# Optimization experiments

Hardware: AMD Instinct MI355X
Metric: run time of the kernel (lower is better)

The kernel has to match this reference:

```python
import jax, jax.numpy as jnp
import numpy as np

B, L = 16384, 32
IN_DIM, TIME_DIM, HIDDEN, HEADS = 128, 64, 256, 4
HEAD_DIM = HIDDEN // HEADS
KV_DIM = IN_DIM + 2 * TIME_DIM
EPS = 1e-5


def setup_inputs() -> dict:
    key = jax.random.key(0)
    ks = jax.random.split(key, 16)
    s = lambda d: 1.0 / np.sqrt(d)
    return {
        "x_u": jax.random.normal(ks[0], (B, IN_DIM), jnp.float32),
        "x_ctx": jax.random.normal(ks[1], (B, L, IN_DIM), jnp.float32),
        "t_ctx": jax.random.uniform(ks[2], (B, L), jnp.float32) * 100.0,
        "freq": jax.random.normal(ks[3], (TIME_DIM,), jnp.float32),
        "phase": jnp.zeros((TIME_DIM,), jnp.float32),
        "Wq": jax.random.normal(ks[4], (IN_DIM, HIDDEN), jnp.float32) * s(IN_DIM),
        "Wk": jax.random.normal(ks[5], (KV_DIM, HIDDEN), jnp.float32) * s(KV_DIM),
        "Wv": jax.random.normal(ks[6], (KV_DIM, HIDDEN), jnp.float32) * s(KV_DIM),
        "Wres": jax.random.normal(ks[7], (IN_DIM, HIDDEN), jnp.float32) * s(IN_DIM),
        "bres": jnp.zeros((HIDDEN,), jnp.float32),
        "W1": jax.random.normal(ks[8], (HIDDEN, HIDDEN), jnp.float32) * s(HIDDEN),
        "b1": jnp.zeros((HIDDEN,), jnp.float32),
        "W2": jax.random.normal(ks[9], (HIDDEN, HIDDEN), jnp.float32) * s(HIDDEN),
        "b2": jnp.zeros((HIDDEN,), jnp.float32),
        "g1": jnp.ones((HIDDEN,), jnp.float32),
        "be1": jnp.zeros((HIDDEN,), jnp.float32),
        "g2": jnp.ones((HIDDEN,), jnp.float32),
        "be2": jnp.zeros((HIDDEN,), jnp.float32),
    }


def _layernorm(x, g, b):
    m = jnp.mean(x, axis=-1, keepdims=True)
    v = jnp.mean((x - m) ** 2, axis=-1, keepdims=True)
    return (x - m) * jax.lax.rsqrt(v + EPS) * g + b


def reference(x_u, x_ctx, t_ctx, freq, phase, Wq, Wk, Wv, Wres, bres,
              W1, b1, W2, b2, g1, be1, g2, be2):
    # --- time encoding: [B, L, 2*TIME_DIM]
    z = jnp.log1p(jnp.maximum(t_ctx, 0.0))[..., None] * freq + phase
    te = jnp.concatenate([jnp.sin(z), jnp.cos(z)], axis=-1)

    # --- single-query multi-head attention over L neighbors
    q = (x_u @ Wq).reshape(B, HEADS, HEAD_DIM)            # [B,H,d]
    kv = jnp.concatenate([x_ctx, te], axis=-1)            # [B,L,KV_DIM]
    k = (kv @ Wk).reshape(B, L, HEADS, HEAD_DIM)          # [B,L,H,d]
    v = (kv @ Wv).reshape(B, L, HEADS, HEAD_DIM)
    att = jnp.einsum('bhd,blhd->bhl', q, k) / np.sqrt(HEAD_DIM)
    att = jax.nn.softmax(att, axis=-1)                    # [B,H,L]
    agg = jnp.einsum('bhl,blhd->bhd', att, v).reshape(B, HIDDEN)

    # --- residual + norms + FFN (dropout is identity in eval)
    z1 = _layernorm(agg + x_u @ Wres + bres, g1, be1)
    ff = jax.nn.relu(z1 @ W1 + b1) @ W2 + b2
    return _layernorm(ff + z1, g2, be2)
```

## Files before the change

### kernel.cpp

```cpp
#include <hip/hip_runtime.h>

typedef unsigned short u16;
typedef unsigned int   u32;

using bf16x8 = __attribute__((ext_vector_type(8))) short;
using f32x4  = __attribute__((ext_vector_type(4))) float;

#define MFMA16(A, B, C) __builtin_amdgcn_mfma_f32_16x16x32_bf16((A), (B), (C), 0, 0, 0)

static __device__ __forceinline__ u16 f2b(float f) {
    u32 u = __builtin_bit_cast(u32, f);
    u32 r = (u + 0x7FFFu + ((u >> 16) & 1u)) >> 16;
    return (u16)r;
}
static __device__ __forceinline__ u16 f2bh(float f) {
    u32 u = __builtin_bit_cast(u32, f) + 0x8000u;
    return (u16)(u >> 16);
}
static __device__ __forceinline__ u32 pk2(float fa, float fb) {
    u32 a = __builtin_bit_cast(u32, fa) + 0x8000u;
    u32 b = __builtin_bit_cast(u32, fb) + 0x8000u;
    return __builtin_amdgcn_perm(b, a, 0x07060302u);
}
static __device__ __forceinline__ bf16x8 cvt8f(f32x4 a, f32x4 b) {
    union { u32 w[4]; bf16x8 v; } r;
    r.w[0] = pk2(a[0], a[1]); r.w[1] = pk2(a[2], a[3]);
    r.w[2] = pk2(b[0], b[1]); r.w[3] = pk2(b[2], b[3]);
    return r.v;
}
static __device__ __forceinline__ bf16x8 cvt8(f32x4 a, f32x4 b) {
    bf16x8 r;
    r[0] = (short)f2b(a[0]); r[1] = (short)f2b(a[1]);
    r[2] = (short)f2b(a[2]); r[3] = (short)f2b(a[3]);
    r[4] = (short)f2b(b[0]); r[5] = (short)f2b(b[1]);
    r[6] = (short)f2b(b[2]); r[7] = (short)f2b(b[3]);
    return r;
}

__global__ __launch_bounds__(256) void k0_prep(
    const float* __restrict__ Wq, const float* __restrict__ Wk,
    const float* __restrict__ Wv, const float* __restrict__ Wres,
    const float* __restrict__ W1, const float* __restrict__ W2,
    u16* __restrict__ WcatT, u16* __restrict__ WresT,
    u16* __restrict__ WvT, u16* __restrict__ W1T, u16* __restrict__ W2T)
{
    int t = blockIdx.x * 256 + threadIdx.x;
    if (t < 131072) {
        int n = t >> 7, i = t & 127;
        int h = n >> 8, c = n & 255;
        const float* wq = Wq + i * 256 + h * 64;
        const float* wk = Wk + c * 256 + h * 64;
        float acc = 0.f;
        #pragma unroll 8
        for (int d = 0; d < 64; ++d) acc += wq[d] * wk[d];
        WcatT[t] = f2b(acc * 0.125f);
    } else if (t < 163840) {
        int o = t - 131072; int n = o >> 7, i = o & 127;
        WresT[o] = f2b(Wres[i * 256 + n]);
    } else if (t < 229376) {
        int o = t - 163840; int n = o >> 8, c = o & 255;
        WvT[o] = f2b(Wv[c * 256 + n]);
    } else if (t < 294912) {
        int o = t - 229376; int n = o >> 8, c = o & 255;
        W1T[o] = f2b(W1[c * 256 + n]);
    } else {
        int o = t - 294912; int n = o >> 8, c = o & 255;
        W2T[o] = f2b(W2[c * 256 + n]);
    }
}

__global__ __launch_bounds__(256) void k1_qkvec(
    const float* __restrict__ xu, const u16* __restrict__ WcatT,
    u16* __restrict__ qkvec)
{
    __shared__ __align__(16) u16 As[128][136];
    const int m0 = blockIdx.x * 128, n0 = blockIdx.y * 128;
    const int t = threadIdx.x;
    #pragma unroll
    for (int i = 0; i < 8; ++i) {
        int c = t + i * 256;
        int row = c >> 4, ch = c & 15;
        const float* src = xu + (size_t)(m0 + row) * 128 + ch * 8;
        f32x4 a = *(const f32x4*)src;
        f32x4 b = *(const f32x4*)(src + 4);
        *(bf16x8*)&As[row][ch * 8] = cvt8(a, b);
    }
    __syncthreads();
    const int lane = t & 63, wave = t >> 6;
    const int quad = lane >> 4, l16 = lane & 15;
    const int mh = (wave >> 1) * 64, nh = (wave & 1) * 64;
    f32x4 zz = {0.f, 0.f, 0.f, 0.f};
    f32x4 acc[4][4];
    #pragma unroll
    for (int mt = 0; mt < 4; ++mt)
        #pragma unroll
        for (int nt = 0; nt < 4; ++nt) acc[mt][nt] = zz;
    #pragma unroll
    for (int ks = 0; ks < 4; ++ks) {
        bf16x8 a[4], b[4];
        #pragma unroll
        for (int mt = 0; mt < 4; ++mt)
            a[mt] = *(const bf16x8*)&As[mh + mt * 16 + l16][ks * 32 + quad * 8];
        #pragma unroll
        for (int nt = 0; nt < 4; ++nt)
            b[nt] = *(const bf16x8*)(WcatT + (size_t)(n0 + nh + nt * 16 + l16) * 128 + ks * 32 + quad * 8);
        #pragma unroll
        for (int mt = 0; mt < 4; ++mt)
            #pragma unroll
            for (int nt = 0; nt < 4; ++nt)
                acc[mt][nt] = MFMA16(a[mt], b[nt], acc[mt][nt]);
    }
    #pragma unroll
    for (int mt = 0; mt < 4; ++mt)
        #pragma unroll
        for (int nt = 0; nt < 4; ++nt) {
            int col = n0 + nh + nt * 16 + l16;
            #pragma unroll
            for (int r = 0; r < 4; ++r) {
                int row = m0 + mh + mt * 16 + quad * 4 + r;
                qkvec[(size_t)row * 1024 + col] = f2b(acc[mt][nt][r]);
            }
        }
}

__global__ __launch_bounds__(256) void k2_attn(
    const float* __restrict__ x_ctx, const float* __restrict__ t_ctx,
    const float* __restrict__ freq, const float* __restrict__ phase,
    u16* __restrict__ qkv)
{
    __shared__ __align__(16) u16 pw[4][4][32];
    const int t = threadIdx.x;
    const int lane = t & 63, wave = t >> 6;
    const int quad = lane >> 4, l16 = lane & 15;
    const int b = blockIdx.x * 4 + wave;
    const int fb = quad * 8;
    const f32x4 zz = {0.f, 0.f, 0.f, 0.f};

    float ltv = log1pf(fmaxf(t_ctx[(size_t)b * 32 + (lane & 31)], 0.f));

    f32x4 fr0a = *(const f32x4*)(freq + fb);
    f32x4 fr0b = *(const f32x4*)(freq + fb + 4);
    f32x4 fr1a = *(const f32x4*)(freq + 32 + fb);
    f32x4 fr1b = *(const f32x4*)(freq + 32 + fb + 4);
    f32x4 ph0a = *(const f32x4*)(phase + fb);
    f32x4 ph0b = *(const f32x4*)(phase + fb + 4);
    f32x4 ph1a = *(const f32x4*)(phase + 32 + fb);
    f32x4 ph1b = *(const f32x4*)(phase + 32 + fb + 4);

    const u16* qb = qkv + (size_t)b * 1024 + (size_t)(l16 & 3) * 256;

    f32x4 accA[2];
    #pragma unroll
    for (int ltile = 0; ltile < 2; ++ltile) {
        const int l = ltile * 16 + l16;
        const float* xrow = x_ctx + ((size_t)b * 32 + l) * 128;
        f32x4 acc = zz;
        #pragma unroll
        for (int ks = 0; ks < 4; ++ks) {
            f32x4 a = *(const f32x4*)(xrow + ks * 32 + fb);
            f32x4 c = *(const f32x4*)(xrow + ks * 32 + fb + 4);
            bf16x8 afr = cvt8f(a, c);
            bf16x8 bfr = *(const bf16x8*)(qb + ks * 32 + fb);
            acc = MFMA16(afr, bfr, acc);
        }
        float lt_l = __shfl(ltv, l);
        f32x4 z0a = fr0a * lt_l + ph0a;
        f32x4 z0b = fr0b * lt_l + ph0b;
        f32x4 z1a = fr1a * lt_l + ph1a;
        f32x4 z1b = fr1b * lt_l + ph1b;
        f32x4 s0a, s0b, s1a, s1b, c0a, c0b, c1a, c1b;
        #pragma unroll
        for (int j = 0; j < 4; ++j) {
            s0a[j] = __sinf(z0a[j]); s0b[j] = __sinf(z0b[j]);
            s1a[j] = __sinf(z1a[j]); s1b[j] = __sinf(z1b[j]);
            c0a[j] = __cosf(z0a[j]); c0b[j] = __cosf(z0b[j]);
            c1a[j] = __cosf(z1a[j]); c1b[j] = __cosf(z1b[j]);
        }
        acc = MFMA16(cvt8f(s0a, s0b), *(const bf16x8*)(qb + 128 + fb), acc);
        acc = MFMA16(cvt8f(s1a, s1b), *(const bf16x8*)(qb + 160 + fb), acc);
        acc = MFMA16(cvt8f(c0a, c0b), *(const bf16x8*)(qb + 192 + fb), acc);
        acc = MFMA16(cvt8f(c1a, c1b), *(const bf16x8*)(qb + 224 + fb), acc);
        accA[ltile] = acc;
    }

    float m = accA[0][0];
    #pragma unroll
    for (int r = 1; r < 4; ++r) m = fmaxf(m, accA[0][r]);
    #pragma unroll
    for (int r = 0; r < 4; ++r) m = fmaxf(m, accA[1][r]);
    m = fmaxf(m, __shfl_xor(m, 16));
    m = fmaxf(m, __shfl_xor(m, 32));
    float p[2][4], s = 0.f;
    #pragma unroll
    for (int lt2 = 0; lt2 < 2; ++lt2)
        #pragma unroll
        for (int r = 0; r < 4; ++r) { p[lt2][r] = __expf(accA[lt2][r] - m); s += p[lt2][r]; }
    s += __shfl_xor(s, 16);
    s += __shfl_xor(s, 32);
    float inv = 1.f / s;
    if (l16 < 4) {
        #pragma unroll
        for (int lt2 = 0; lt2 < 2; ++lt2)
            #pragma unroll
            for (int r = 0; r < 4; ++r)
                pw[wave][l16][lt2 * 16 + quad * 4 + r] = f2bh(p[lt2][r] * inv);
    }
    __syncthreads();

    bf16x8 pfr = *(const bf16x8*)&pw[wave][l16 & 3][fb];
    float ltj[8];
    #pragma unroll
    for (int j = 0; j < 8; ++j) ltj[j] = __shfl(ltv, fb + j);

    u16* crow = qkv + (size_t)b * 1024;
    #pragma unroll
    for (int nt = 0; nt < 8; ++nt) {
        int c = nt * 16 + l16;
        const float* xp = x_ctx + ((size_t)b * 32 + fb) * 128 + c;
        float v0 = xp[0], v1 = xp[128], v2 = xp[256], v3 = xp[384];
        float v4 = xp[512], v5 = xp[640], v6 = xp[768], v7 = xp[896];
        union { u32 w[4]; bf16x8 v; } bu;
        bu.w[0] = pk2(v0, v1); bu.w[1] = pk2(v2, v3);
        bu.w[2] = pk2(v4, v5); bu.w[3] = pk2(v6, v7);
        f32x4 d = MFMA16(pfr, bu.v, zz);
        if (quad == 0) {
            #pragma unroll
            for (int r = 0; r < 4; ++r) crow[r * 256 + c] = f2bh(d[r]);
        }
    }
    #pragma unroll
    for (int pp = 0; pp < 4; ++pp) {
        int f = pp * 16 + l16;
        float fq = freq[f], phf = phase[f];
        float z8[8];
        #pragma unroll
        for (int j = 0; j < 8; ++j) z8[j] = ltj[j] * fq + phf;
        union { u32 w[4]; bf16x8 v; } bs, bc;
        #pragma unroll
        for (int j = 0; j < 4; ++j) {
            bs.w[j] = pk2(__sinf(z8[2 * j]), __sinf(z8[2 * j + 1]));
            bc.w[j] = pk2(__cosf(z8[2 * j]), __cosf(z8[2 * j + 1]));
        }
        f32x4 ds = MFMA16(pfr, bs.v, zz);
        f32x4 dc = MFMA16(pfr, bc.v, zz);
        if (quad == 0) {
            #pragma unroll
            for (int r = 0; r < 4; ++r) {
                crow[r * 256 + 128 + f] = f2bh(ds[r]);
                crow[r * 256 + 192 + f] = f2bh(dc[r]);
            }
        }
    }
}

__global__ __launch_bounds__(256) void k3_epilogue(
    const u16* __restrict__ ctxb, const float* __restrict__ xu,
    const u16* __restrict__ WvT, const u16* __restrict__ WresT,
    const u16* __restrict__ W1T, const u16* __restrict__ W2T,
    const float* __restrict__ bres, const float* __restrict__ b1,
    const float* __restrict__ b2, const float* __restrict__ g1,
    const float* __restrict__ be1, const float* __restrict__ g2,
    const float* __restrict__ be2, float* __restrict__ out)
{
    __shared__ __align__(16) char smem[39552];
    u16  (*ctxs)[1032] = reinterpret_cast<u16 (*)[1032]>(smem);
    u16  (*xus)[136]   = reinterpret_cast<u16 (*)[136]>(smem + 33024);
    float(*zbuf)[264]  = reinterpret_cast<float (*)[264]>(smem);
    u16  (*z1b)[264]   = reinterpret_cast<u16 (*)[264]>(smem + 16896);
    u16  (*h1b)[264]   = reinterpret_cast<u16 (*)[264]>(smem + 25344);
    float(*obuf)[264]  = reinterpret_cast<float (*)[264]>(smem + 16896);
    float(*red)[16][2] = reinterpret_cast<float (*)[16][2]>(smem + 37376);
    float(*mrstd)[2]   = reinterpret_cast<float (*)[2]>(smem + 39424);

    const int b0 = blockIdx.x * 16;
    const int t = threadIdx.x;
    const int lane = t & 63, wave = t >> 6;
    const int quad = lane >> 4, l16 = lane & 15;
    const int nw = wave * 64;

    #pragma unroll
    for (int i = 0; i < 8; ++i) {
        int idx = t + i * 256;
        int row = idx >> 7, ch = idx & 127;
        *(bf16x8*)&ctxs[row][ch * 8] = *(const bf16x8*)(ctxb + (size_t)(b0 + row) * 1024 + ch * 8);
    }
    {
        int row = t >> 4, ch = t & 15;
        const float* src = xu + (size_t)(b0 + row) * 128 + ch * 8;
        f32x4 a = *(const f32x4*)src;
        f32x4 b = *(const f32x4*)(src + 4);
        *(bf16x8*)&xus[row][ch * 8] = cvt8(a, b);
    }
    __syncthreads();

    f32x4 zz = {0.f, 0.f, 0.f, 0.f};

    f32x4 acc[4];
    #pragma unroll
    for (int nt = 0; nt < 4; ++nt) acc[nt] = zz;
    #pragma unroll
    for (int ks = 0; ks < 8; ++ks) {
        bf16x8 afr = *(const bf16x8*)&ctxs[l16][wave * 256 + ks * 32 + quad * 8];
        #pragma unroll
        for (int nt = 0; nt < 4; ++nt) {
            bf16x8 bfr = *(const bf16x8*)(WvT + (size_t)(nw + nt * 16 + l16) * 256 + ks * 32 + quad * 8);
            acc[nt] = MFMA16(afr, bfr, acc[nt]);
        }
    }
    #pragma unroll
    for (int ks = 0; ks < 4; ++ks) {
        bf16x8 afr = *(const bf16x8*)&xus[l16][ks * 32 + quad * 8];
        #pragma unroll
        for (int nt = 0; nt < 4; ++nt) {
            bf16x8 bfr = *(const bf16x8*)(WresT + (size_t)(nw + nt * 16 + l16) * 128 + ks * 32 + quad * 8);
            acc[nt] = MFMA16(afr, bfr, acc[nt]);
        }
    }
    __syncthreads();
    #pragma unroll
    for (int nt = 0; nt < 4; ++nt) {
        int col = nw + nt * 16 + l16;
        float bb = bres[col];
        #pragma unroll
        for (int r = 0; r < 4; ++r)
            zbuf[quad * 4 + r][col] = acc[nt][r] + bb;
    }
    __syncthreads();

    {
        int row = t >> 4, j = t & 15;
        float s = 0.f, s2 = 0.f;
        #pragma unroll
        for (int i = 0; i < 16; ++i) { float v = zbuf[row][j + 16 * i]; s += v; s2 += v * v; }
        red[row][j][0] = s; red[row][j][1] = s2;
    }
    __syncthreads();
    if (t < 16) {
        float s = 0.f, s2 = 0.f;
        #pragma unroll
        for (int j = 0; j < 16; ++j) { s += red[t][j][0]; s2 += red[t][j][1]; }
        float m = s * (1.f / 256.f);
        float var = s2 * (1.f / 256.f) - m * m;
        mrstd[t][0] = m;
        mrstd[t][1] = rsqrtf(var + 1e-5f);
    }
    __syncthreads();
    {
        float g = g1[t], be = be1[t];
        #pragma unroll
        for (int i = 0; i < 16; ++i) {
            float z = (zbuf[i][t] - mrstd[i][0]) * mrstd[i][1] * g + be;
            zbuf[i][t] = z;
            z1b[i][t] = f2b(z);
        }
    }
    __syncthreads();

    f32x4 acc2[4];
    #pragma unroll
    for (int nt = 0; nt < 4; ++nt) acc2[nt] = zz;
    #pragma unroll
    for (int ks = 0; ks < 8; ++ks) {
        bf16x8 afr = *(const bf16x8*)&z1b[l16][ks * 32 + quad * 8];
        #pragma unroll
        for (int nt = 0; nt < 4; ++nt) {
            bf16x8 bfr = *(const bf16x8*)(W1T + (size_t)(nw + nt * 16 + l16) * 256 + ks * 32 + quad * 8);
            acc2[nt] = MFMA16(afr, bfr, acc2[nt]);
        }
    }
    #pragma unroll
    for (int nt = 0; nt < 4; ++nt) {
        int col = nw + nt * 16 + l16;
        float bb = b1[col];
        #pragma unroll
        for (int r = 0; r < 4; ++r)
            h1b[quad * 4 + r][col] = f2b(fmaxf(acc2[nt][r] + bb, 0.f));
    }
    __syncthreads();

    f32x4 acc3[4];
    #pragma unroll
    for (int nt = 0; nt < 4; ++nt) acc3[nt] = zz;
    #pragma unroll
    for (int ks = 0; ks < 8; ++ks) {
        bf16x8 afr = *(const bf16x8*)&h1b[l16][ks * 32 + quad * 8];
        #pragma unroll
        for (int nt = 0; nt < 4; ++nt) {
            bf16x8 bfr = *(const bf16x8*)(W2T + (size_t)(nw + nt * 16 + l16) * 256 + ks * 32 + quad * 8);
            acc3[nt] = MFMA16(afr, bfr, acc3[nt]);
        }
    }
    __syncthreads();
    #pragma unroll
    for (int nt = 0; nt < 4; ++nt) {
        int col = nw + nt * 16 + l16;
        float bb = b2[col];
        #pragma unroll
        for (int r = 0; r < 4; ++r) {
            int row = quad * 4 + r;
            obuf[row][col] = acc3[nt][r] + bb + zbuf[row][col];
        }
    }
    __syncthreads();

    {
        int row = t >> 4, j = t & 15;
        float s = 0.f, s2 = 0.f;
        #pragma unroll
        for (int i = 0; i < 16; ++i) { float v = obuf[row][j + 16 * i]; s += v; s2 += v * v; }
        red[row][j][0] = s; red[row][j][1] = s2;
    }
    __syncthreads();
    if (t < 16) {
        float s = 0.f, s2 = 0.f;
        #pragma unroll
        for (int j = 0; j < 16; ++j) { s += red[t][j][0]; s2 += red[t][j][1]; }
        float m = s * (1.f / 256.f);
        float var = s2 * (1.f / 256.f) - m * m;
        mrstd[t][0] = m;
        mrstd[t][1] = rsqrtf(var + 1e-5f);
    }
    __syncthreads();
    {
        float g = g2[t], be = be2[t];
        #pragma unroll
        for (int i = 0; i < 16; ++i)
            out[(size_t)(b0 + i) * 256 + t] = (obuf[i][t] - mrstd[i][0]) * mrstd[i][1] * g + be;
    }
}

extern "C" void kernel_launch(void* const* d_in, const int* in_sizes, int n_in,
                              void* d_out, int out_size, void* d_ws, size_t ws_size,
                              hipStream_t stream)
{
    (void)in_sizes; (void)n_in; (void)out_size; (void)ws_size;
    const float* xu    = (const float*)d_in[0];
    const float* x_ctx = (const float*)d_in[1];
    const float* t_ctx = (const float*)d_in[2];
    const float* freq  = (const float*)d_in[3];
    const float* phase = (const float*)d_in[4];
    const float* Wq    = (const float*)d_in[5];
    const float* Wk    = (const float*)d_in[6];
    const float* Wv    = (const float*)d_in[7];
    const float* Wres  = (const float*)d_in[8];
    const float* bres  = (const float*)d_in[9];
    const float* W1    = (const float*)d_in[10];
    const float* b1    = (const float*)d_in[11];
    const float* W2    = (const float*)d_in[12];
    const float* b2    = (const float*)d_in[13];
    const float* g1    = (const float*)d_in[14];
    const float* be1   = (const float*)d_in[15];
    const float* g2    = (const float*)d_in[16];
    const float* be2   = (const float*)d_in[17];
    float* out = (float*)d_out;

    char* ws = (char*)d_ws;
    u16* qkv   = (u16*)(ws);
    u16* WcatT = (u16*)(ws + 33554432);
    u16* WresT = (u16*)(ws + 33816576);
    u16* WvT   = (u16*)(ws + 33882112);
    u16* W1T   = (u16*)(ws + 34013184);
    u16* W2T   = (u16*)(ws + 34144256);

    hipLaunchKernelGGL(k0_prep, dim3(1408), dim3(256), 0, stream,
                       Wq, Wk, Wv, Wres, W1, W2, WcatT, WresT, WvT, W1T, W2T);
    hipLaunchKernelGGL(k1_qkvec, dim3(128, 8), dim3(256), 0, stream,
                       xu, WcatT, qkv);
    hipLaunchKernelGGL(k2_attn, dim3(4096), dim3(256), 0, stream,
                       x_ctx, t_ctx, freq, phase, qkv);
    hipLaunchKernelGGL(k3_epilogue, dim3(1024), dim3(256), 0, stream,
                       qkv, xu, WvT, WresT, W1T, W2T,
                       bres, b1, b2, g1, be1, g2, be2, out);
}
```

Baseline: 502.9 us.

## Fuse q-projection, attention, and epilogue kernels into one per-block kernel

Merges the q·Wk projection, the attention/context kernel and the epilogue into a single kernel. Each block handles 16 batch rows and keeps the per-row qk vectors and attention contexts in shared memory instead of writing them to and reading them back from a 32 MB global workspace. This removes two kernel launches and the global round-trip of the intermediate buffer. In exchange there are fewer blocks (1024 instead of 4096) for the memory-bound x_ctx streaming phase, each wave now loops over 4 rows with a block-wide barrier per iteration, and the shared-memory footprint grows.

```diff
diff --git a/kernel.cpp b/kernel.cpp
--- a/kernel.cpp
+++ b/kernel.cpp
@@ -69,74 +69,59 @@
     }
 }
 
-__global__ __launch_bounds__(256) void k1_qkvec(
-    const float* __restrict__ xu, const u16* __restrict__ WcatT,
-    u16* __restrict__ qkvec)
+__global__ __launch_bounds__(256, 4) void kf_fused(
+    const float* __restrict__ xu, const float* __restrict__ x_ctx,
+    const float* __restrict__ t_ctx, const float* __restrict__ freq,
+    const float* __restrict__ phase,
+    const u16* __restrict__ WcatT, const u16* __restrict__ WvT,
+    const u16* __restrict__ WresT, const u16* __restrict__ W1T,
+    const u16* __restrict__ W2T,
+    const float* __restrict__ bres, const float* __restrict__ b1,
+    const float* __restrict__ b2, const float* __restrict__ g1,
+    const float* __restrict__ be1, const float* __restrict__ g2,
+    const float* __restrict__ be2, float* __restrict__ out)
 {
-    __shared__ __align__(16) u16 As[128][136];
-    const int m0 = blockIdx.x * 128, n0 = blockIdx.y * 128;
-    const int t = threadIdx.x;
-    #pragma unroll
-    for (int i = 0; i < 8; ++i) {
-        int c = t + i * 256;
-        int row = c >> 4, ch = c & 15;
-        const float* src = xu + (size_t)(m0 + row) * 128 + ch * 8;
-        f32x4 a = *(const f32x4*)src;
-        f32x4 b = *(const f32x4*)(src + 4);
-        *(bf16x8*)&As[row][ch * 8] = cvt8(a, b);
-    }
-    __syncthreads();
-    const int lane = t & 63, wave = t >> 6;
-    const int quad = lane >> 4, l16 = lane & 15;
-    const int mh = (wave >> 1) * 64, nh = (wave & 1) * 64;
-    f32x4 zz = {0.f, 0.f, 0.f, 0.f};
-    f32x4 acc[4][4];
-    #pragma unroll
-    for (int mt = 0; mt < 4; ++mt)
-        #pragma unroll
-        for (int nt = 0; nt < 4; ++nt) acc[mt][nt] = zz;
-    #pragma unroll
-    for (int ks = 0; ks < 4; ++ks) {
-        bf16x8 a[4], b[4];
-        #pragma unroll
-        for (int mt = 0; mt < 4; ++mt)
-            a[mt] = *(const bf16x8*)&As[mh + mt * 16 + l16][ks * 32 + quad * 8];
-        #pragma unroll
-        for (int nt = 0; nt < 4; ++nt)
-            b[nt] = *(const bf16x8*)(WcatT + (size_t)(n0 + nh + nt * 16 + l16) * 128 + ks * 32 + quad * 8);
-        #pragma unroll
-        for (int mt = 0; mt < 4; ++mt)
-            #pragma unroll
-            for (int nt = 0; nt < 4; ++nt)
-                acc[mt][nt] = MFMA16(a[mt], b[nt], acc[mt][nt]);
-    }
-    #pragma unroll
-    for (int mt = 0; mt < 4; ++mt)
-        #pragma unroll
-        for (int nt = 0; nt < 4; ++nt) {
-            int col = n0 + nh + nt * 16 + l16;
-            #pragma unroll
-            for (int r = 0; r < 4; ++r) {
-                int row = m0 + mh + mt * 16 + quad * 4 + r;
-                qkvec[(size_t)row * 1024 + col] = f2b(acc[mt][nt][r]);
-            }
-        }
-}
-
-__global__ __launch_bounds__(256) void k2_attn(
-    const float* __restrict__ x_ctx, const float* __restrict__ t_ctx,
-    const float* __restrict__ freq, const float* __restrict__ phase,
-    u16* __restrict__ qkv)
-{
-    __shared__ __align__(16) u16 pw[4][4][32];
+    __shared__ __align__(16) char smem[40576];
+    u16  (*kv)[1032]   = reinterpret_cast<u16 (*)[1032]>(smem);
+    u16  (*xus)[136]   = reinterpret_cast<u16 (*)[136]>(smem + 33024);
+    u16  (*pw)[4][32]  = reinterpret_cast<u16 (*)[4][32]>(smem + 37376);
+    float(*red)[16][2] = reinterpret_cast<float (*)[16][2]>(smem + 38400);
+    float(*mrstd)[2]   = reinterpret_cast<float (*)[2]>(smem + 40448);
+    float(*zbuf)[264]  = reinterpret_cast<float (*)[264]>(smem);
+    u16  (*z1b)[264]   = reinterpret_cast<u16 (*)[264]>(smem + 16896);
+    u16  (*h1b)[264]   = reinterpret_cast<u16 (*)[264]>(smem + 25344);
+    float(*obuf)[264]  = reinterpret_cast<float (*)[264]>(smem + 16896);
+
+    const int b0 = blockIdx.x * 16;
     const int t = threadIdx.x;
     const int lane = t & 63, wave = t >> 6;
     const int quad = lane >> 4, l16 = lane & 15;
-    const int b = blockIdx.x * 4 + wave;
     const int fb = quad * 8;
+    const int nw = wave * 64;
     const f32x4 zz = {0.f, 0.f, 0.f, 0.f};
 
-    float ltv = log1pf(fmaxf(t_ctx[(size_t)b * 32 + (lane & 31)], 0.f));
+    {
+        int row = t >> 4, ch = t & 15;
+        const float* src = xu + (size_t)(b0 + row) * 128 + ch * 8;
+        *(bf16x8*)&xus[row][ch * 8] = cvt8(*(const f32x4*)src, *(const f32x4*)(src + 4));
+    }
+    __syncthreads();
+
+    #pragma unroll 4
+    for (int nt = 0; nt < 16; ++nt) {
+        int n0 = wave * 256 + nt * 16;
+        f32x4 acc = zz;
+        #pragma unroll
+        for (int ks = 0; ks < 4; ++ks) {
+            bf16x8 afr = *(const bf16x8*)&xus[l16][ks * 32 + fb];
+            bf16x8 bfr = *(const bf16x8*)(WcatT + (size_t)(n0 + l16) * 128 + ks * 32 + fb);
+            acc = MFMA16(afr, bfr, acc);
+        }
+        #pragma unroll
+        for (int r = 0; r < 4; ++r)
+            kv[quad * 4 + r][n0 + l16] = f2b(acc[r]);
+    }
+    __syncthreads();
 
     f32x4 fr0a = *(const f32x4*)(freq + fb);
     f32x4 fr0b = *(const f32x4*)(freq + fb + 4);
@@ -147,160 +132,120 @@
     f32x4 ph1a = *(const f32x4*)(phase + 32 + fb);
     f32x4 ph1b = *(const f32x4*)(phase + 32 + fb + 4);
 
-    const u16* qb = qkv + (size_t)b * 1024 + (size_t)(l16 & 3) * 256;
-
-    f32x4 accA[2];
-    #pragma unroll
-    for (int ltile = 0; ltile < 2; ++ltile) {
-        const int l = ltile * 16 + l16;
-        const float* xrow = x_ctx + ((size_t)b * 32 + l) * 128;
-        f32x4 acc = zz;
-        #pragma unroll
-        for (int ks = 0; ks < 4; ++ks) {
-            f32x4 a = *(const f32x4*)(xrow + ks * 32 + fb);
-            f32x4 c = *(const f32x4*)(xrow + ks * 32 + fb + 4);
-            bf16x8 afr = cvt8f(a, c);
-            bf16x8 bfr = *(const bf16x8*)(qb + ks * 32 + fb);
-            acc = MFMA16(afr, bfr, acc);
-        }
-        float lt_l = __shfl(ltv, l);
-        f32x4 z0a = fr0a * lt_l + ph0a;
-        f32x4 z0b = fr0b * lt_l + ph0b;
-        f32x4 z1a = fr1a * lt_l + ph1a;
-        f32x4 z1b = fr1b * lt_l + ph1b;
-        f32x4 s0a, s0b, s1a, s1b, c0a, c0b, c1a, c1b;
-        #pragma unroll
-        for (int j = 0; j < 4; ++j) {
-            s0a[j] = __sinf(z0a[j]); s0b[j] = __sinf(z0b[j]);
-            s1a[j] = __sinf(z1a[j]); s1b[j] = __sinf(z1b[j]);
-            c0a[j] = __cosf(z0a[j]); c0b[j] = __cosf(z0b[j]);
-            c1a[j] = __cosf(z1a[j]); c1b[j] = __cosf(z1b[j]);
-        }
-        acc = MFMA16(cvt8f(s0a, s0b), *(const bf16x8*)(qb + 128 + fb), acc);
-        acc = MFMA16(cvt8f(s1a, s1b), *(const bf16x8*)(qb + 160 + fb), acc);
-        acc = MFMA16(cvt8f(c0a, c0b), *(const bf16x8*)(qb + 192 + fb), acc);
-        acc = MFMA16(cvt8f(c1a, c1b), *(const bf16x8*)(qb + 224 + fb), acc);
-        accA[ltile] = acc;
-    }
-
-    float m = accA[0][0];
-    #pragma unroll
-    for (int r = 1; r < 4; ++r) m = fmaxf(m, accA[0][r]);
-    #pragma unroll
-    for (int r = 0; r < 4; ++r) m = fmaxf(m, accA[1][r]);
-    m = fmaxf(m, __shfl_xor(m, 16));
-    m = fmaxf(m, __shfl_xor(m, 32));
-    float p[2][4], s = 0.f;
-    #pragma unroll
-    for (int lt2 = 0; lt2 < 2; ++lt2)
-        #pragma unroll
-        for (int r = 0; r < 4; ++r) { p[lt2][r] = __expf(accA[lt2][r] - m); s += p[lt2][r]; }
-    s += __shfl_xor(s, 16);
-    s += __shfl_xor(s, 32);
-    float inv = 1.f / s;
-    if (l16 < 4) {
+    for (int i = 0; i < 4; ++i) {
+        const int kvrow = wave * 4 + i;
+        const int b = b0 + kvrow;
+        float ltv = log1pf(fmaxf(t_ctx[(size_t)b * 32 + (lane & 31)], 0.f));
+        const u16* qb = &kv[kvrow][(l16 & 3) * 256];
+
+        f32x4 accA[2];
+        #pragma unroll
+        for (int ltile = 0; ltile < 2; ++ltile) {
+            const int l = ltile * 16 + l16;
+            const float* xrow = x_ctx + ((size_t)b * 32 + l) * 128;
+            f32x4 acc = zz;
+            #pragma unroll
+            for (int ks = 0; ks < 4; ++ks) {
+                f32x4 a = *(const f32x4*)(xrow + ks * 32 + fb);
+                f32x4 c = *(const f32x4*)(xrow + ks * 32 + fb + 4);
+                acc = MFMA16(cvt8f(a, c), *(const bf16x8*)(qb + ks * 32 + fb), acc);
+            }
+            float lt_l = __shfl(ltv, l);
+            f32x4 z0a = fr0a * lt_l + ph0a;
+            f32x4 z0b = fr0b * lt_l + ph0b;
+            f32x4 z1a = fr1a * lt_l + ph1a;
+            f32x4 z1b_ = fr1b * lt_l + ph1b;
+            f32x4 s0a, s0b, s1a, s1b, c0a, c0b, c1a, c1b;
+            #pragma unroll
+            for (int j = 0; j < 4; ++j) {
+                s0a[j] = __sinf(z0a[j]); s0b[j] = __sinf(z0b[j]);
+                s1a[j] = __sinf(z1a[j]); s1b[j] = __sinf(z1b_[j]);
+                c0a[j] = __cosf(z0a[j]); c0b[j] = __cosf(z0b[j]);
+                c1a[j] = __cosf(z1a[j]); c1b[j] = __cosf(z1b_[j]);
+            }
+            acc = MFMA16(cvt8f(s0a, s0b), *(const bf16x8*)(qb + 128 + fb), acc);
+            acc = MFMA16(cvt8f(s1a, s1b), *(const bf16x8*)(qb + 160 + fb), acc);
+            acc = MFMA16(cvt8f(c0a, c0b), *(const bf16x8*)(qb + 192 + fb), acc);
+            acc = MFMA16(cvt8f(c1a, c1b), *(const bf16x8*)(qb + 224 + fb), acc);
+            accA[ltile] = acc;
+        }
+
+        float m = accA[0][0];
+        #pragma unroll
+        for (int r = 1; r < 4; ++r) m = fmaxf(m, accA[0][r]);
+        #pragma unroll
+        for (int r = 0; r < 4; ++r) m = fmaxf(m, accA[1][r]);
+        m = fmaxf(m, __shfl_xor(m, 16));
+        m = fmaxf(m, __shfl_xor(m, 32));
+        float p[2][4], s = 0.f;
         #pragma unroll
         for (int lt2 = 0; lt2 < 2; ++lt2)
             #pragma unroll
-            for (int r = 0; r < 4; ++r)
-                pw[wave][l16][lt2 * 16 + quad * 4 + r] = f2bh(p[lt2][r] * inv);
-    }
-    __syncthreads();
-
-    bf16x8 pfr = *(const bf16x8*)&pw[wave][l16 & 3][fb];
-    float ltj[8];
-    #pragma unroll
-    for (int j = 0; j < 8; ++j) ltj[j] = __shfl(ltv, fb + j);
-
-    u16* crow = qkv + (size_t)b * 1024;
-    #pragma unroll
-    for (int nt = 0; nt < 8; ++nt) {
-        int c = nt * 16 + l16;
-        const float* xp = x_ctx + ((size_t)b * 32 + fb) * 128 + c;
-        float v0 = xp[0], v1 = xp[128], v2 = xp[256], v3 = xp[384];
-        float v4 = xp[512], v5 = xp[640], v6 = xp[768], v7 = xp[896];
-        union { u32 w[4]; bf16x8 v; } bu;
-        bu.w[0] = pk2(v0, v1); bu.w[1] = pk2(v2, v3);
-        bu.w[2] = pk2(v4, v5); bu.w[3] = pk2(v6, v7);
-        f32x4 d = MFMA16(pfr, bu.v, zz);
-        if (quad == 0) {
-            #pragma unroll
-            for (int r = 0; r < 4; ++r) crow[r * 256 + c] = f2bh(d[r]);
-        }
-    }
-    #pragma unroll
-    for (int pp = 0; pp < 4; ++pp) {
-        int f = pp * 16 + l16;
-        float fq = freq[f], phf = phase[f];
-        float z8[8];
-        #pragma unroll
-        for (int j = 0; j < 8; ++j) z8[j] = ltj[j] * fq + phf;
-        union { u32 w[4]; bf16x8 v; } bs, bc;
-        #pragma unroll
-        for (int j = 0; j < 4; ++j) {
-            bs.w[j] = pk2(__sinf(z8[2 * j]), __sinf(z8[2 * j + 1]));
-            bc.w[j] = pk2(__cosf(z8[2 * j]), __cosf(z8[2 * j + 1]));
-        }
-        f32x4 ds = MFMA16(pfr, bs.v, zz);
-        f32x4 dc = MFMA16(pfr, bc.v, zz);
-        if (quad == 0) {
-            #pragma unroll
-            for (int r = 0; r < 4; ++r) {
-                crow[r * 256 + 128 + f] = f2bh(ds[r]);
-                crow[r * 256 + 192 + f] = f2bh(dc[r]);
+            for (int r = 0; r < 4; ++r) { p[lt2][r] = __expf(accA[lt2][r] - m); s += p[lt2][r]; }
+        s += __shfl_xor(s, 16);
+        s += __shfl_xor(s, 32);
+        float inv = 1.f / s;
+        if (l16 < 4) {
+            #pragma unroll
+            for (int lt2 = 0; lt2 < 2; ++lt2)
+                #pragma unroll
+                for (int r = 0; r < 4; ++r)
+                    pw[wave][l16][lt2 * 16 + quad * 4 + r] = f2bh(p[lt2][r] * inv);
+        }
+        __syncthreads();
+
+        bf16x8 pfr = *(const bf16x8*)&pw[wave][l16 & 3][fb];
+        float ltj[8];
+        #pragma unroll
+        for (int j = 0; j < 8; ++j) ltj[j] = __shfl(ltv, fb + j);
+
+        #pragma unroll
+        for (int nt = 0; nt < 8; ++nt) {
+            int c = nt * 16 + l16;
+            const float* xp = x_ctx + ((size_t)b * 32 + fb) * 128 + c;
+            float v0 = xp[0], v1 = xp[128], v2 = xp[256], v3 = xp[384];
+            float v4 = xp[512], v5 = xp[640], v6 = xp[768], v7 = xp[896];
+            union { u32 w[4]; bf16x8 v; } bu;
+            bu.w[0] = pk2(v0, v1); bu.w[1] = pk2(v2, v3);
+            bu.w[2] = pk2(v4, v5); bu.w[3] = pk2(v6, v7);
+            f32x4 d = MFMA16(pfr, bu.v, zz);
+            if (quad == 0) {
+                #pragma unroll
+                for (int r = 0; r < 4; ++r) kv[kvrow][r * 256 + c] = f2bh(d[r]);
             }
         }
-    }
-}
-
-__global__ __launch_bounds__(256) void k3_epilogue(
-    const u16* __restrict__ ctxb, const float* __restrict__ xu,
-    const u16* __restrict__ WvT, const u16* __restrict__ WresT,
-    const u16* __restrict__ W1T, const u16* __restrict__ W2T,
-    const float* __restrict__ bres, const float* __restrict__ b1,
-    const float* __restrict__ b2, const float* __restrict__ g1,
-    const float* __restrict__ be1, const float* __restrict__ g2,
-    const float* __restrict__ be2, float* __restrict__ out)
-{
-    __shared__ __align__(16) char smem[39552];
-    u16  (*ctxs)[1032] = reinterpret_cast<u16 (*)[1032]>(smem);
-    u16  (*xus)[136]   = reinterpret_cast<u16 (*)[136]>(smem + 33024);
-    float(*zbuf)[264]  = reinterpret_cast<float (*)[264]>(smem);
-    u16  (*z1b)[264]   = reinterpret_cast<u16 (*)[264]>(smem + 16896);
-    u16  (*h1b)[264]   = reinterpret_cast<u16 (*)[264]>(smem + 25344);
-    float(*obuf)[264]  = reinterpret_cast<float (*)[264]>(smem + 16896);
-    float(*red)[16][2] = reinterpret_cast<float (*)[16][2]>(smem + 37376);
-    float(*mrstd)[2]   = reinterpret_cast<float (*)[2]>(smem + 39424);
-
-    const int b0 = blockIdx.x * 16;
-    const int t = threadIdx.x;
-    const int lane = t & 63, wave = t >> 6;
-    const int quad = lane >> 4, l16 = lane & 15;
-    const int nw = wave * 64;
-
-    #pragma unroll
-    for (int i = 0; i < 8; ++i) {
-        int idx = t + i * 256;
-        int row = idx >> 7, ch = idx & 127;
-        *(bf16x8*)&ctxs[row][ch * 8] = *(const bf16x8*)(ctxb + (size_t)(b0 + row) * 1024 + ch * 8);
-    }
-    {
-        int row = t >> 4, ch = t & 15;
-        const float* src = xu + (size_t)(b0 + row) * 128 + ch * 8;
-        f32x4 a = *(const f32x4*)src;
-        f32x4 b = *(const f32x4*)(src + 4);
-        *(bf16x8*)&xus[row][ch * 8] = cvt8(a, b);
-    }
-    __syncthreads();
-
-    f32x4 zz = {0.f, 0.f, 0.f, 0.f};
+        #pragma unroll
+        for (int pp = 0; pp < 4; ++pp) {
+            int f = pp * 16 + l16;
+            float fq = freq[f], phf = phase[f];
+            float z8[8];
+            #pragma unroll
+            for (int j = 0; j < 8; ++j) z8[j] = ltj[j] * fq + phf;
+            union { u32 w[4]; bf16x8 v; } bs, bc;
+            #pragma unroll
+            for (int j = 0; j < 4; ++j) {
+                bs.w[j] = pk2(__sinf(z8[2 * j]), __sinf(z8[2 * j + 1]));
+                bc.w[j] = pk2(__cosf(z8[2 * j]), __cosf(z8[2 * j + 1]));
+            }
+            f32x4 ds = MFMA16(pfr, bs.v, zz);
+            f32x4 dc = MFMA16(pfr, bc.v, zz);
+            if (quad == 0) {
+                #pragma unroll
+                for (int r = 0; r < 4; ++r) {
+                    kv[kvrow][r * 256 + 128 + f] = f2bh(ds[r]);
+                    kv[kvrow][r * 256 + 192 + f] = f2bh(dc[r]);
+                }
+            }
+        }
+    }
+    __syncthreads();
 
     f32x4 acc[4];
     #pragma unroll
     for (int nt = 0; nt < 4; ++nt) acc[nt] = zz;
     #pragma unroll
     for (int ks = 0; ks < 8; ++ks) {
-        bf16x8 afr = *(const bf16x8*)&ctxs[l16][wave * 256 + ks * 32 + quad * 8];
+        bf16x8 afr = *(const bf16x8*)&kv[l16][wave * 256 + ks * 32 + quad * 8];
         #pragma unroll
         for (int nt = 0; nt < 4; ++nt) {
             bf16x8 bfr = *(const bf16x8*)(WvT + (size_t)(nw + nt * 16 + l16) * 256 + ks * 32 + quad * 8);
@@ -331,7 +276,7 @@
         int row = t >> 4, j = t & 15;
         float s = 0.f, s2 = 0.f;
         #pragma unroll
-        for (int i = 0; i < 16; ++i) { float v = zbuf[row][j + 16 * i]; s += v; s2 += v * v; }
+        for (int i2 = 0; i2 < 16; ++i2) { float v = zbuf[row][j + 16 * i2]; s += v; s2 += v * v; }
         red[row][j][0] = s; red[row][j][1] = s2;
     }
     __syncthreads();
@@ -348,10 +293,10 @@
     {
         float g = g1[t], be = be1[t];
         #pragma unroll
-        for (int i = 0; i < 16; ++i) {
-            float z = (zbuf[i][t] - mrstd[i][0]) * mrstd[i][1] * g + be;
-            zbuf[i][t] = z;
-            z1b[i][t] = f2b(z);
+        for (int i2 = 0; i2 < 16; ++i2) {
+            float z = (zbuf[i2][t] - mrstd[i2][0]) * mrstd[i2][1] * g + be;
+            zbuf[i2][t] = z;
+            z1b[i2][t] = f2b(z);
         }
     }
     __syncthreads();
@@ -407,7 +352,7 @@
         int row = t >> 4, j = t & 15;
         float s = 0.f, s2 = 0.f;
         #pragma unroll
-        for (int i = 0; i < 16; ++i) { float v = obuf[row][j + 16 * i]; s += v; s2 += v * v; }
+        for (int i2 = 0; i2 < 16; ++i2) { float v = obuf[row][j + 16 * i2]; s += v; s2 += v * v; }
         red[row][j][0] = s; red[row][j][1] = s2;
     }
     __syncthreads();
@@ -424,8 +369,8 @@
     {
         float g = g2[t], be = be2[t];
         #pragma unroll
-        for (int i = 0; i < 16; ++i)
-            out[(size_t)(b0 + i) * 256 + t] = (obuf[i][t] - mrstd[i][0]) * mrstd[i][1] * g + be;
+        for (int i2 = 0; i2 < 16; ++i2)
+            out[(size_t)(b0 + i2) * 256 + t] = (obuf[i2][t] - mrstd[i2][0]) * mrstd[i2][1] * g + be;
     }
 }
 
@@ -455,20 +400,16 @@
     float* out = (float*)d_out;
 
     char* ws = (char*)d_ws;
-    u16* qkv   = (u16*)(ws);
-    u16* WcatT = (u16*)(ws + 33554432);
-    u16* WresT = (u16*)(ws + 33816576);
-    u16* WvT   = (u16*)(ws + 33882112);
-    u16* W1T   = (u16*)(ws + 34013184);
-    u16* W2T   = (u16*)(ws + 34144256);
+    u16* WcatT = (u16*)(ws);
+    u16* WresT = (u16*)(ws + 262144);
+    u16* WvT   = (u16*)(ws + 327680);
+    u16* W1T   = (u16*)(ws + 458752);
+    u16* W2T   = (u16*)(ws + 589824);
 
     hipLaunchKernelGGL(k0_prep, dim3(1408), dim3(256), 0, stream,
                        Wq, Wk, Wv, Wres, W1, W2, WcatT, WresT, WvT, W1T, W2T);
-    hipLaunchKernelGGL(k1_qkvec, dim3(128, 8), dim3(256), 0, stream,
-                       xu, WcatT, qkv);
-    hipLaunchKernelGGL(k2_attn, dim3(4096), dim3(256), 0, stream,
-                       x_ctx, t_ctx, freq, phase, qkv);
-    hipLaunchKernelGGL(k3_epilogue, dim3(1024), dim3(256), 0, stream,
-                       qkv, xu, WvT, WresT, W1T, W2T,
+    hipLaunchKernelGGL(kf_fused, dim3(1024), dim3(256), 0, stream,
+                       xu, x_ctx, t_ctx, freq, phase,
+                       WcatT, WvT, WresT, W1T, W2T,
                        bres, b1, b2, g1, be1, g2, be2, out);
 }
```

Result: no change. 501.0 us (-0.4%).
